# Kernel tuning notes

Measured on AMD Instinct MI355X. Metric: run time of the kernel, lower is better.

Reference implementation:

```python
import jax, jax.numpy as jnp
import numpy as np

N_GROUPS = 4
N_LIMITED_GROUPS = 2
TOP_K = 2
ROUTE_SCALE = 1.0


def setup_inputs() -> dict:
    key = jax.random.key(0)
    k1, k2, k3, k4 = jax.random.split(key, 4)
    n_tokens, dim, n_experts = 65536, 4096, 16
    return {
        "x": jax.random.normal(k1, (n_tokens, dim), dtype=jnp.float32),
        "w1_weight": jax.random.normal(k2, (n_experts, dim), dtype=jnp.float32) * 0.02,
        "w1_bias": jax.random.normal(k3, (n_experts,), dtype=jnp.float32) * 0.02,
        "route_bias": jax.random.normal(k4, (n_experts,), dtype=jnp.float32) * 0.02,
    }


def reference(x, w1_weight, w1_bias, route_bias):
    # Linear scorer: [N, E]
    logits = x @ w1_weight.T + w1_bias
    # softmax in fp32 (score_func == 'softmax')
    scores = jax.nn.softmax(logits.astype(jnp.float32), axis=-1)
    # bias add (moe_use_bias=True); original_scores includes the bias
    scores = scores + route_bias
    original_scores = scores

    n = x.shape[0]
    # group masking: view [N, n_groups, experts_per_group]
    g = scores.reshape(n, N_GROUPS, -1)
    group_scores = g.max(axis=-1)  # amax path since bias is not None
    _, gidx = jax.lax.top_k(group_scores, N_LIMITED_GROUPS)  # [N, n_limited]
    keep = jnp.zeros((n, N_GROUPS), dtype=bool).at[
        jnp.arange(n)[:, None], gidx
    ].set(True)
    masked = jnp.where(keep[:, :, None], g, -jnp.inf).reshape(n, -1)

    # top-k over masked scores; gather values from original (unmasked-at-topk) scores
    _, indices = jax.lax.top_k(masked, TOP_K)  # [N, k]
    values = jnp.take_along_axis(original_scores, indices, axis=1) * ROUTE_SCALE
    return values.astype(x.dtype), indices
```

## Files before the change

### kernel.cpp

```cpp
#include <hip/hip_runtime.h>
#include <math.h>

constexpr int NE  = 16;
constexpr int NG  = 4;
constexpr int NSL = 4;
constexpr int KS  = 16;
constexpr int TPB = 128;
#define MARGIN 1e-4

__global__ __launch_bounds__(256)
void w_transpose_kernel(const float* __restrict__ w, float* __restrict__ wt,
                        int dim, int n) {
    int id = blockIdx.x * 256 + threadIdx.x;
    if (id < n) {
        int k = id / NE;
        int e = id - k * NE;
        wt[id] = w[(size_t)e * dim + k];
    }
}

struct RouteR { double v1, v2; int i1, i2; double mg, mo, ms; };

__device__ __forceinline__ RouteR route_epilogue(const double* tot,
                                                 const float* w1b,
                                                 const float* rbias)
{
    double logit[NE];
    double m = -INFINITY;
#pragma unroll
    for (int e = 0; e < NE; ++e) {
        logit[e] = tot[e] + (double)w1b[e];
        m = fmax(m, logit[e]);
    }
    double ssum = 0.0, p[NE];
#pragma unroll
    for (int e = 0; e < NE; ++e) { p[e] = exp(logit[e] - m); ssum += p[e]; }
    double inv = 1.0 / ssum, sc[NE];
#pragma unroll
    for (int e = 0; e < NE; ++e) sc[e] = p[e] * inv + (double)rbias[e];

    double gm[NG];
#pragma unroll
    for (int g = 0; g < NG; ++g) {
        double a = fmax(sc[g * 4 + 0], sc[g * 4 + 1]);
        double b = fmax(sc[g * 4 + 2], sc[g * 4 + 3]);
        gm[g] = fmax(a, b);
    }
    int g1 = 0;
#pragma unroll
    for (int g = 1; g < NG; ++g) if (gm[g] > gm[g1]) g1 = g;
    int g2 = (g1 == 0) ? 1 : 0;
#pragma unroll
    for (int g = 0; g < NG; ++g) if (g != g1 && gm[g] > gm[g2]) g2 = g;
    double gm3 = -INFINITY;
#pragma unroll
    for (int g = 0; g < NG; ++g)
        if (g != g1 && g != g2 && gm[g] > gm3) gm3 = gm[g];

    RouteR r;
    r.v1 = -INFINITY; r.i1 = 0;
#pragma unroll
    for (int e = 0; e < NE; ++e) {
        int g = e >> 2;
        bool keep = (g == g1) || (g == g2);
        if (keep && sc[e] > r.v1) { r.v1 = sc[e]; r.i1 = e; }
    }
    r.v2 = -INFINITY; r.i2 = 0;
#pragma unroll
    for (int e = 0; e < NE; ++e) {
        int g = e >> 2;
        bool keep = ((g == g1) || (g == g2)) && (e != r.i1);
        if (keep && sc[e] > r.v2) { r.v2 = sc[e]; r.i2 = e; }
    }
    double v3 = -INFINITY;
#pragma unroll
    for (int e = 0; e < NE; ++e) {
        int g = e >> 2;
        bool keep = ((g == g1) || (g == g2)) && (e != r.i1) && (e != r.i2);
        if (keep && sc[e] > v3) v3 = sc[e];
    }
    r.mg = gm[g2] - gm3;
    r.mo = r.v1 - r.v2;
    r.ms = r.v2 - v3;
    return r;
}

__global__ __launch_bounds__(256)
void k1_main(const float* __restrict__ x,
             const float* __restrict__ wt,
             const float* __restrict__ w1b,
             const float* __restrict__ rbias,
             float* __restrict__ dout,
             int* __restrict__ fcount,
             int* __restrict__ flist,
             int n_tokens, int dim)
{
    __shared__ float wbuf[NSL][KS][NE];
    __shared__ float red[NSL - 1][2][64][NE + 1];

    const int tid  = threadIdx.x;
    const int uwid = __builtin_amdgcn_readfirstlane(tid >> 6);
    const int lane = tid & 63;
    const int slice = dim / NSL;
    const int nst  = slice / KS;
    const long tokA = (long)blockIdx.x * TPB + lane;
    const long tokB = tokA + 64;

    const float* xA = x + tokA * (size_t)dim + (size_t)uwid * slice;
    const float* xB = x + tokB * (size_t)dim + (size_t)uwid * slice;
    const float* wp = wt + (size_t)uwid * slice * NE;

    float accA[NE], accB[NE];
#pragma unroll
    for (int e = 0; e < NE; ++e) { accA[e] = 0.f; accB[e] = 0.f; }

    float4 a0 = *(const float4*)(xA + 0),  a1 = *(const float4*)(xA + 4);
    float4 a2 = *(const float4*)(xA + 8),  a3 = *(const float4*)(xA + 12);
    float4 b0 = *(const float4*)(xB + 0),  b1 = *(const float4*)(xB + 4);
    float4 b2 = *(const float4*)(xB + 8),  b3 = *(const float4*)(xB + 12);
    float4 wreg = *(const float4*)(wp + lane * 4);

    for (int c = 0; c < nst; ++c) {
        ((float4*)&wbuf[uwid][0][0])[lane] = wreg;

        float4 na0 = a0, na1 = a1, na2 = a2, na3 = a3;
        float4 nb0 = b0, nb1 = b1, nb2 = b2, nb3 = b3;
        if (c + 1 < nst) {
            const float* pa = xA + (c + 1) * KS;
            const float* pb = xB + (c + 1) * KS;
            na0 = *(const float4*)(pa + 0);  na1 = *(const float4*)(pa + 4);
            na2 = *(const float4*)(pa + 8);  na3 = *(const float4*)(pa + 12);
            nb0 = *(const float4*)(pb + 0);  nb1 = *(const float4*)(pb + 4);
            nb2 = *(const float4*)(pb + 8);  nb3 = *(const float4*)(pb + 12);
            wreg = *(const float4*)(wp + (size_t)(c + 1) * KS * NE + lane * 4);
        }

        float fa[KS], fb[KS];
        fa[0]=a0.x;  fa[1]=a0.y;  fa[2]=a0.z;  fa[3]=a0.w;
        fa[4]=a1.x;  fa[5]=a1.y;  fa[6]=a1.z;  fa[7]=a1.w;
        fa[8]=a2.x;  fa[9]=a2.y;  fa[10]=a2.z; fa[11]=a2.w;
        fa[12]=a3.x; fa[13]=a3.y; fa[14]=a3.z; fa[15]=a3.w;
        fb[0]=b0.x;  fb[1]=b0.y;  fb[2]=b0.z;  fb[3]=b0.w;
        fb[4]=b1.x;  fb[5]=b1.y;  fb[6]=b1.z;  fb[7]=b1.w;
        fb[8]=b2.x;  fb[9]=b2.y;  fb[10]=b2.z; fb[11]=b2.w;
        fb[12]=b3.x; fb[13]=b3.y; fb[14]=b3.z; fb[15]=b3.w;

#pragma unroll
        for (int kk = 0; kk < KS; ++kk) {
            float xa_ = fa[kk];
            float xb_ = fb[kk];
#pragma unroll
            for (int eg = 0; eg < 4; ++eg) {
                float4 wv = *(const float4*)&wbuf[uwid][kk][eg * 4];
                accA[eg*4+0] = fmaf(xa_, wv.x, accA[eg*4+0]);
                accA[eg*4+1] = fmaf(xa_, wv.y, accA[eg*4+1]);
                accA[eg*4+2] = fmaf(xa_, wv.z, accA[eg*4+2]);
                accA[eg*4+3] = fmaf(xa_, wv.w, accA[eg*4+3]);
                accB[eg*4+0] = fmaf(xb_, wv.x, accB[eg*4+0]);
                accB[eg*4+1] = fmaf(xb_, wv.y, accB[eg*4+1]);
                accB[eg*4+2] = fmaf(xb_, wv.z, accB[eg*4+2]);
                accB[eg*4+3] = fmaf(xb_, wv.w, accB[eg*4+3]);
            }
        }

        a0=na0; a1=na1; a2=na2; a3=na3;
        b0=nb0; b1=nb1; b2=nb2; b3=nb3;
    }

    if (uwid != 0) {
#pragma unroll
        for (int e = 0; e < NE; ++e) {
            red[uwid - 1][0][lane][e] = accA[e];
            red[uwid - 1][1][lane][e] = accB[e];
        }
    }
    __syncthreads();
    if (uwid != 0) return;

#pragma unroll
    for (int t = 0; t < 2; ++t) {
        double tot[NE];
#pragma unroll
        for (int e = 0; e < NE; ++e) {
            float a = (t == 0) ? accA[e] : accB[e];
            tot[e] = (((double)a + (double)red[0][t][lane][e])
                      + (double)red[1][t][lane][e]) + (double)red[2][t][lane][e];
        }
        RouteR r = route_epilogue(tot, w1b, rbias);
        long tok = (t == 0) ? tokA : tokB;

        double mmin = fmin(r.mg, fmin(r.mo, r.ms));
        if (mmin < MARGIN) {
            int idx = atomicAdd(fcount, 1);
            if (idx < n_tokens) flist[idx] = (int)tok;
        }
        float2 vv; vv.x = (float)r.v1; vv.y = (float)r.v2;
        *(float2*)(dout + tok * 2) = vv;
        float2 iv; iv.x = (float)r.i1; iv.y = (float)r.i2;
        *(float2*)(dout + (long)n_tokens * 2 + tok * 2) = iv;
    }
}

__global__ __launch_bounds__(256)
void k2_recheck(const float* __restrict__ x,
                const float* __restrict__ wt,
                const float* __restrict__ w1b,
                const float* __restrict__ rbias,
                float* __restrict__ dout,
                const int* __restrict__ fcount,
                const int* __restrict__ flist,
                int n_tokens, int dim)
{
    const int tid  = threadIdx.x;
    const int lane = tid & 63;
    const int wavesPerBlock = blockDim.x >> 6;
    const int wglobal = blockIdx.x * wavesPerBlock + (tid >> 6);
    const int nwaves  = gridDim.x * wavesPerBlock;
    int nf = *fcount;
    if (nf > n_tokens) nf = n_tokens;
    const int nq = dim / 256;

    for (int i = wglobal; i < nf; i += nwaves) {
        const int t = flist[i];
        const float* xr = x + (size_t)t * dim;

        double part[NE];
#pragma unroll
        for (int e = 0; e < NE; ++e) part[e] = 0.0;

        for (int q = 0; q < nq; ++q) {
            float4 xv = *(const float4*)(xr + q * 256 + lane * 4);
#pragma unroll
            for (int j = 0; j < 4; ++j) {
                int k = q * 256 + lane * 4 + j;
                double xd = (double)((const float*)&xv)[j];
                const float* wr = wt + (size_t)k * NE;
#pragma unroll
                for (int e = 0; e < NE; ++e)
                    part[e] = fma(xd, (double)wr[e], part[e]);
            }
        }

#pragma unroll
        for (int off = 1; off < 64; off <<= 1) {
#pragma unroll
            for (int e = 0; e < NE; ++e)
                part[e] += __shfl_xor(part[e], off, 64);
        }

        RouteR r = route_epilogue(part, w1b, rbias);
        if (lane == 0) {
            float2 vv; vv.x = (float)r.v1; vv.y = (float)r.v2;
            *(float2*)(dout + (long)t * 2) = vv;
            float2 iv; iv.x = (float)r.i1; iv.y = (float)r.i2;
            *(float2*)(dout + (long)n_tokens * 2 + (long)t * 2) = iv;
        }
    }
}

__global__ __launch_bounds__(256)
void router_fallback(const float* __restrict__ x,
                     const float* __restrict__ w1w,
                     const float* __restrict__ w1b,
                     const float* __restrict__ rbias,
                     float* __restrict__ dout,
                     int n_tokens, int dim)
{
    __shared__ double wbuf4[4][16][NE];
    const int tid  = threadIdx.x;
    const int uwid = __builtin_amdgcn_readfirstlane(tid >> 6);
    const int lane = tid & 63;
    const int slice = dim / 4;
    const int nst  = slice / 16;
    const long tokA = (long)blockIdx.x * 128 + lane;
    const long tokB = tokA + 64;
    const float* xA = x + tokA * (size_t)dim + (size_t)uwid * slice;
    const float* xB = x + tokB * (size_t)dim + (size_t)uwid * slice;

    double accA[NE], accB[NE];
#pragma unroll
    for (int e = 0; e < NE; ++e) { accA[e] = 0.0; accB[e] = 0.0; }

    float4 a0 = *(const float4*)(xA + 0), a1 = *(const float4*)(xA + 4);
    float4 a2 = *(const float4*)(xA + 8), a3 = *(const float4*)(xA + 12);
    float4 b0 = *(const float4*)(xB + 0), b1 = *(const float4*)(xB + 4);
    float4 b2 = *(const float4*)(xB + 8), b3 = *(const float4*)(xB + 12);
    float4 wreg;
    {
        const int i0 = lane * 4;
#pragma unroll
        for (int j = 0; j < 4; ++j) {
            int i = i0 + j;
            ((float*)&wreg)[j] = w1w[(size_t)(i & 15) * dim + uwid * slice + (i >> 4)];
        }
    }

    for (int c = 0; c < nst; ++c) {
        {
            double* dst = &wbuf4[uwid][0][0] + lane * 4;
            dst[0] = (double)wreg.x;  dst[1] = (double)wreg.y;
            dst[2] = (double)wreg.z;  dst[3] = (double)wreg.w;
        }
        float4 na0=a0,na1=a1,na2=a2,na3=a3,nb0=b0,nb1=b1,nb2=b2,nb3=b3;
        if (c + 1 < nst) {
            const float* pa = xA + (c + 1) * 16;
            const float* pb = xB + (c + 1) * 16;
            na0 = *(const float4*)(pa + 0);  na1 = *(const float4*)(pa + 4);
            na2 = *(const float4*)(pa + 8);  na3 = *(const float4*)(pa + 12);
            nb0 = *(const float4*)(pb + 0);  nb1 = *(const float4*)(pb + 4);
            nb2 = *(const float4*)(pb + 8);  nb3 = *(const float4*)(pb + 12);
            const int kb = uwid * slice + (c + 1) * 16;
            const int i0 = lane * 4;
#pragma unroll
            for (int j = 0; j < 4; ++j) {
                int i = i0 + j;
                ((float*)&wreg)[j] = w1w[(size_t)(i & 15) * dim + kb + (i >> 4)];
            }
        }
        float fa[16], fb[16];
        fa[0]=a0.x; fa[1]=a0.y; fa[2]=a0.z; fa[3]=a0.w;
        fa[4]=a1.x; fa[5]=a1.y; fa[6]=a1.z; fa[7]=a1.w;
        fa[8]=a2.x; fa[9]=a2.y; fa[10]=a2.z; fa[11]=a2.w;
        fa[12]=a3.x; fa[13]=a3.y; fa[14]=a3.z; fa[15]=a3.w;
        fb[0]=b0.x; fb[1]=b0.y; fb[2]=b0.z; fb[3]=b0.w;
        fb[4]=b1.x; fb[5]=b1.y; fb[6]=b1.z; fb[7]=b1.w;
        fb[8]=b2.x; fb[9]=b2.y; fb[10]=b2.z; fb[11]=b2.w;
        fb[12]=b3.x; fb[13]=b3.y; fb[14]=b3.z; fb[15]=b3.w;
#pragma unroll
        for (int kk = 0; kk < 16; ++kk) {
            double xa_ = (double)fa[kk];
            double xb_ = (double)fb[kk];
#pragma unroll
            for (int ep = 0; ep < NE / 2; ++ep) {
                double2 wv = *(const double2*)&wbuf4[uwid][kk][ep * 2];
                accA[ep*2+0] = fma(xa_, wv.x, accA[ep*2+0]);
                accA[ep*2+1] = fma(xa_, wv.y, accA[ep*2+1]);
                accB[ep*2+0] = fma(xb_, wv.x, accB[ep*2+0]);
                accB[ep*2+1] = fma(xb_, wv.y, accB[ep*2+1]);
            }
        }
        a0=na0; a1=na1; a2=na2; a3=na3;
        b0=nb0; b1=nb1; b2=nb2; b3=nb3;
    }

    __syncthreads();
    __shared__ double red[3][2][64][NE + 1];
    if (uwid != 0) {
#pragma unroll
        for (int e = 0; e < NE; ++e) {
            red[uwid - 1][0][lane][e] = accA[e];
            red[uwid - 1][1][lane][e] = accB[e];
        }
    }
    __syncthreads();
    if (uwid != 0) return;

#pragma unroll
    for (int t = 0; t < 2; ++t) {
        double tot[NE];
#pragma unroll
        for (int e = 0; e < NE; ++e) {
            double a = (t == 0) ? accA[e] : accB[e];
            tot[e] = ((a + red[0][t][lane][e]) + red[1][t][lane][e])
                     + red[2][t][lane][e];
        }
        RouteR r = route_epilogue(tot, w1b, rbias);
        long tok = (t == 0) ? tokA : tokB;
        float2 vv; vv.x = (float)r.v1; vv.y = (float)r.v2;
        *(float2*)(dout + tok * 2) = vv;
        float2 iv; iv.x = (float)r.i1; iv.y = (float)r.i2;
        *(float2*)(dout + (long)n_tokens * 2 + tok * 2) = iv;
    }
}

extern "C" void kernel_launch(void* const* d_in, const int* in_sizes, int n_in,
                              void* d_out, int out_size, void* d_ws, size_t ws_size,
                              hipStream_t stream)
{
    const float* x   = (const float*)d_in[0];
    const float* w1w = (const float*)d_in[1];
    const float* w1b = (const float*)d_in[2];
    const float* rb  = (const float*)d_in[3];
    float* out = (float*)d_out;

    const int ne       = in_sizes[2];
    const int dim      = in_sizes[1] / ne;
    const int n_tokens = in_sizes[0] / dim;

    const int nW = dim * ne;
    const size_t WT_BYTES  = (size_t)nW * sizeof(float);
    const size_t COUNT_OFF = WT_BYTES;
    const size_t LIST_OFF  = WT_BYTES + 128;
    const size_t need = LIST_OFF + (size_t)n_tokens * sizeof(int);

    if (ws_size >= need) {
        float* wt    = (float*)d_ws;
        int* fcount  = (int*)((char*)d_ws + COUNT_OFF);
        int* flist   = (int*)((char*)d_ws + LIST_OFF);

        hipMemsetAsync(fcount, 0, sizeof(int), stream);
        hipLaunchKernelGGL(w_transpose_kernel, dim3((nW + 255) / 256), dim3(256),
                           0, stream, w1w, wt, dim, nW);
        hipLaunchKernelGGL(k1_main, dim3(n_tokens / TPB), dim3(NSL * 64),
                           0, stream, x, wt, w1b, rb, out, fcount, flist,
                           n_tokens, dim);
        hipLaunchKernelGGL(k2_recheck, dim3(256), dim3(256),
                           0, stream, x, wt, w1b, rb, out, fcount, flist,
                           n_tokens, dim);
    } else {
        hipLaunchKernelGGL(router_fallback, dim3(n_tokens / 128), dim3(256),
                           0, stream, x, w1w, w1b, rb, out, n_tokens, dim);
    }
}
```

Baseline: 314.9 us.

## Compute router logits with split-bf16 MFMA instead of fp32 FMA

Replaces the scalar fp32 FMA main kernel with one that uses the bf16 matrix-core instruction 16x16x32. Both x and the weights are split into hi/lo bf16 parts and combined with three MFMAs to approximate fp32 accuracy. The weight prep kernel now also writes the hi/lo bf16 copies. Each wave handles 16 tokens over the full K dimension, which removes the cross-wave split-K reduction. The main cost targeted is ALU throughput of the FMA loop, but the kernel reads 262144x... of x, so it may be bandwidth bound. Accuracy loss is meant to be covered by the existing margin-based recheck kernel, which may now flag more tokens.

```diff
diff --git a/kernel.cpp b/kernel.cpp
--- a/kernel.cpp
+++ b/kernel.cpp
@@ -1,21 +1,33 @@
 #include <hip/hip_runtime.h>
 #include <math.h>
 
-constexpr int NE  = 16;
-constexpr int NG  = 4;
-constexpr int NSL = 4;
-constexpr int KS  = 16;
-constexpr int TPB = 128;
+constexpr int NE = 16;
+constexpr int NG = 4;
 #define MARGIN 1e-4
 
+typedef __attribute__((ext_vector_type(8))) short bf16x8;
+typedef __attribute__((ext_vector_type(4))) float f32x4;
+
+__device__ __forceinline__ unsigned short f2bf_rne(float f) {
+    unsigned u = __float_as_uint(f);
+    unsigned r = (u + 0x7fffu + ((u >> 16) & 1u)) >> 16;
+    return (unsigned short)r;
+}
+
 __global__ __launch_bounds__(256)
-void w_transpose_kernel(const float* __restrict__ w, float* __restrict__ wt,
-                        int dim, int n) {
+void w_prep_kernel(const float* __restrict__ w, float* __restrict__ wt,
+                   unsigned short* __restrict__ whi, unsigned short* __restrict__ wlo,
+                   int dim, int n) {
     int id = blockIdx.x * 256 + threadIdx.x;
     if (id < n) {
-        int k = id / NE;
-        int e = id - k * NE;
-        wt[id] = w[(size_t)e * dim + k];
+        int e = id / dim;
+        int k = id - e * dim;
+        float f = w[id];
+        wt[(size_t)k * NE + e] = f;
+        unsigned short h = f2bf_rne(f);
+        float back = __uint_as_float(((unsigned)h) << 16);
+        whi[id] = h;
+        wlo[id] = f2bf_rne(f - back);
     }
 }
 
@@ -86,8 +98,9 @@
 }
 
 __global__ __launch_bounds__(256)
-void k1_main(const float* __restrict__ x,
-             const float* __restrict__ wt,
+void k1_mfma(const float* __restrict__ x,
+             const unsigned short* __restrict__ whi,
+             const unsigned short* __restrict__ wlo,
              const float* __restrict__ w1b,
              const float* __restrict__ rbias,
              float* __restrict__ dout,
@@ -95,99 +108,65 @@
              int* __restrict__ flist,
              int n_tokens, int dim)
 {
-    __shared__ float wbuf[NSL][KS][NE];
-    __shared__ float red[NSL - 1][2][64][NE + 1];
-
+    __shared__ float scl[4][16][NE + 1];
     const int tid  = threadIdx.x;
-    const int uwid = __builtin_amdgcn_readfirstlane(tid >> 6);
+    const int wid  = tid >> 6;
     const int lane = tid & 63;
-    const int slice = dim / NSL;
-    const int nst  = slice / KS;
-    const long tokA = (long)blockIdx.x * TPB + lane;
-    const long tokB = tokA + 64;
-
-    const float* xA = x + tokA * (size_t)dim + (size_t)uwid * slice;
-    const float* xB = x + tokB * (size_t)dim + (size_t)uwid * slice;
-    const float* wp = wt + (size_t)uwid * slice * NE;
-
-    float accA[NE], accB[NE];
-#pragma unroll
-    for (int e = 0; e < NE; ++e) { accA[e] = 0.f; accB[e] = 0.f; }
-
-    float4 a0 = *(const float4*)(xA + 0),  a1 = *(const float4*)(xA + 4);
-    float4 a2 = *(const float4*)(xA + 8),  a3 = *(const float4*)(xA + 12);
-    float4 b0 = *(const float4*)(xB + 0),  b1 = *(const float4*)(xB + 4);
-    float4 b2 = *(const float4*)(xB + 8),  b3 = *(const float4*)(xB + 12);
-    float4 wreg = *(const float4*)(wp + lane * 4);
+    const int m    = lane & 15;
+    const int kg   = lane >> 4;
+    const long tok0 = (long)blockIdx.x * 64 + wid * 16;
+    const int nst = dim / 32;
+
+    const float* xp = x + (tok0 + m) * (size_t)dim + kg * 8;
+    const unsigned short* whp = whi + (size_t)m * dim + kg * 8;
+    const unsigned short* wlp = wlo + (size_t)m * dim + kg * 8;
+
+    f32x4 acc = {0.f, 0.f, 0.f, 0.f};
+
+    float4 xa = *(const float4*)(xp);
+    float4 xb = *(const float4*)(xp + 4);
+    bf16x8 wh = *(const bf16x8*)(whp);
+    bf16x8 wl = *(const bf16x8*)(wlp);
 
     for (int c = 0; c < nst; ++c) {
-        ((float4*)&wbuf[uwid][0][0])[lane] = wreg;
-
-        float4 na0 = a0, na1 = a1, na2 = a2, na3 = a3;
-        float4 nb0 = b0, nb1 = b1, nb2 = b2, nb3 = b3;
+        float4 nxa = xa, nxb = xb;
+        bf16x8 nwh = wh, nwl = wl;
         if (c + 1 < nst) {
-            const float* pa = xA + (c + 1) * KS;
-            const float* pb = xB + (c + 1) * KS;
-            na0 = *(const float4*)(pa + 0);  na1 = *(const float4*)(pa + 4);
-            na2 = *(const float4*)(pa + 8);  na3 = *(const float4*)(pa + 12);
-            nb0 = *(const float4*)(pb + 0);  nb1 = *(const float4*)(pb + 4);
-            nb2 = *(const float4*)(pb + 8);  nb3 = *(const float4*)(pb + 12);
-            wreg = *(const float4*)(wp + (size_t)(c + 1) * KS * NE + lane * 4);
-        }
-
-        float fa[KS], fb[KS];
-        fa[0]=a0.x;  fa[1]=a0.y;  fa[2]=a0.z;  fa[3]=a0.w;
-        fa[4]=a1.x;  fa[5]=a1.y;  fa[6]=a1.z;  fa[7]=a1.w;
-        fa[8]=a2.x;  fa[9]=a2.y;  fa[10]=a2.z; fa[11]=a2.w;
-        fa[12]=a3.x; fa[13]=a3.y; fa[14]=a3.z; fa[15]=a3.w;
-        fb[0]=b0.x;  fb[1]=b0.y;  fb[2]=b0.z;  fb[3]=b0.w;
-        fb[4]=b1.x;  fb[5]=b1.y;  fb[6]=b1.z;  fb[7]=b1.w;
-        fb[8]=b2.x;  fb[9]=b2.y;  fb[10]=b2.z; fb[11]=b2.w;
-        fb[12]=b3.x; fb[13]=b3.y; fb[14]=b3.z; fb[15]=b3.w;
-
-#pragma unroll
-        for (int kk = 0; kk < KS; ++kk) {
-            float xa_ = fa[kk];
-            float xb_ = fb[kk];
-#pragma unroll
-            for (int eg = 0; eg < 4; ++eg) {
-                float4 wv = *(const float4*)&wbuf[uwid][kk][eg * 4];
-                accA[eg*4+0] = fmaf(xa_, wv.x, accA[eg*4+0]);
-                accA[eg*4+1] = fmaf(xa_, wv.y, accA[eg*4+1]);
-                accA[eg*4+2] = fmaf(xa_, wv.z, accA[eg*4+2]);
-                accA[eg*4+3] = fmaf(xa_, wv.w, accA[eg*4+3]);
-                accB[eg*4+0] = fmaf(xb_, wv.x, accB[eg*4+0]);
-                accB[eg*4+1] = fmaf(xb_, wv.y, accB[eg*4+1]);
-                accB[eg*4+2] = fmaf(xb_, wv.z, accB[eg*4+2]);
-                accB[eg*4+3] = fmaf(xb_, wv.w, accB[eg*4+3]);
-            }
-        }
-
-        a0=na0; a1=na1; a2=na2; a3=na3;
-        b0=nb0; b1=nb1; b2=nb2; b3=nb3;
-    }
-
-    if (uwid != 0) {
-#pragma unroll
-        for (int e = 0; e < NE; ++e) {
-            red[uwid - 1][0][lane][e] = accA[e];
-            red[uwid - 1][1][lane][e] = accB[e];
-        }
-    }
-    __syncthreads();
-    if (uwid != 0) return;
-
-#pragma unroll
-    for (int t = 0; t < 2; ++t) {
+            const float* xn = xp + (size_t)(c + 1) * 32;
+            nxa = *(const float4*)(xn);
+            nxb = *(const float4*)(xn + 4);
+            nwh = *(const bf16x8*)(whp + (size_t)(c + 1) * 32);
+            nwl = *(const bf16x8*)(wlp + (size_t)(c + 1) * 32);
+        }
+
+        float xf[8] = {xa.x, xa.y, xa.z, xa.w, xb.x, xb.y, xb.z, xb.w};
+        bf16x8 xhi, xlo;
+#pragma unroll
+        for (int j = 0; j < 8; ++j) {
+            float f = xf[j];
+            unsigned short h = f2bf_rne(f);
+            float back = __uint_as_float(((unsigned)h) << 16);
+            xhi[j] = (short)h;
+            xlo[j] = (short)f2bf_rne(f - back);
+        }
+
+        acc = __builtin_amdgcn_mfma_f32_16x16x32_bf16(xhi, wh, acc, 0, 0, 0);
+        acc = __builtin_amdgcn_mfma_f32_16x16x32_bf16(xlo, wh, acc, 0, 0, 0);
+        acc = __builtin_amdgcn_mfma_f32_16x16x32_bf16(xhi, wl, acc, 0, 0, 0);
+
+        xa = nxa; xb = nxb; wh = nwh; wl = nwl;
+    }
+
+#pragma unroll
+    for (int j = 0; j < 4; ++j)
+        scl[wid][kg * 4 + j][m] = acc[j];
+
+    if (lane < 16) {
         double tot[NE];
 #pragma unroll
-        for (int e = 0; e < NE; ++e) {
-            float a = (t == 0) ? accA[e] : accB[e];
-            tot[e] = (((double)a + (double)red[0][t][lane][e])
-                      + (double)red[1][t][lane][e]) + (double)red[2][t][lane][e];
-        }
+        for (int e = 0; e < NE; ++e) tot[e] = (double)scl[wid][lane][e];
         RouteR r = route_epilogue(tot, w1b, rbias);
-        long tok = (t == 0) ? tokA : tokB;
+        long tok = tok0 + lane;
 
         double mmin = fmin(r.mg, fmin(r.mo, r.ms));
         if (mmin < MARGIN) {
@@ -389,20 +368,24 @@
 
     const int nW = dim * ne;
     const size_t WT_BYTES  = (size_t)nW * sizeof(float);
-    const size_t COUNT_OFF = WT_BYTES;
-    const size_t LIST_OFF  = WT_BYTES + 128;
+    const size_t WHI_OFF   = WT_BYTES;
+    const size_t WLO_OFF   = WHI_OFF + (size_t)nW * 2;
+    const size_t COUNT_OFF = WLO_OFF + (size_t)nW * 2;
+    const size_t LIST_OFF  = COUNT_OFF + 128;
     const size_t need = LIST_OFF + (size_t)n_tokens * sizeof(int);
 
     if (ws_size >= need) {
-        float* wt    = (float*)d_ws;
-        int* fcount  = (int*)((char*)d_ws + COUNT_OFF);
-        int* flist   = (int*)((char*)d_ws + LIST_OFF);
+        float* wt            = (float*)d_ws;
+        unsigned short* whi  = (unsigned short*)((char*)d_ws + WHI_OFF);
+        unsigned short* wlo  = (unsigned short*)((char*)d_ws + WLO_OFF);
+        int* fcount          = (int*)((char*)d_ws + COUNT_OFF);
+        int* flist           = (int*)((char*)d_ws + LIST_OFF);
 
         hipMemsetAsync(fcount, 0, sizeof(int), stream);
-        hipLaunchKernelGGL(w_transpose_kernel, dim3((nW + 255) / 256), dim3(256),
-                           0, stream, w1w, wt, dim, nW);
-        hipLaunchKernelGGL(k1_main, dim3(n_tokens / TPB), dim3(NSL * 64),
-                           0, stream, x, wt, w1b, rb, out, fcount, flist,
+        hipLaunchKernelGGL(w_prep_kernel, dim3((nW + 255) / 256), dim3(256),
+                           0, stream, w1w, wt, whi, wlo, dim, nW);
+        hipLaunchKernelGGL(k1_mfma, dim3(n_tokens / 64), dim3(256),
+                           0, stream, x, whi, wlo, w1b, rb, out, fcount, flist,
                            n_tokens, dim);
         hipLaunchKernelGGL(k2_recheck, dim3(256), dim3(256),
                            0, stream, x, wt, w1b, rb, out, fcount, flist,
```

Measured after the change: 323.2 us. 1.03x slower.
